# Performance work log

Measured on AMD Instinct MI355X. Metric: run time of the kernel, lower is better.

## Reference

```python
import jax, jax.numpy as jnp
import numpy as np

N = 4194304  # data_size
EPS = 1e-12  # torch f.normalize eps


def setup_inputs() -> dict:
    key = jax.random.key(0)
    k1, = jax.random.split(key, 1)
    inputs = jax.random.normal(k1, (N, 3, 3), dtype=jnp.float32)
    kd = jnp.zeros((3,), dtype=jnp.float32)   # nn.Parameter([0,0,0])
    ks = jnp.ones((3,), dtype=jnp.float32)    # nn.Parameter([1,1,1])
    p = jnp.float32(16.0)                     # nn.Parameter(16.0)
    return {"inputs": inputs, "kd": kd, "ks": ks, "p": p}


def reference(inputs, kd, ks, p):
    # inputs: [N, 3, 3] -> light, normal, view each [N, 3]
    light = inputs[:, 0, :]
    normal = inputs[:, 1, :]
    view = inputs[:, 2, :]
    intensity = jnp.float32(1.0)

    # diffuse: kd * intensity * max(0, dot(light, normal))  -> [N, 1] * [3]
    ln = jnp.maximum(0.0, jnp.sum(light * normal, axis=-1, keepdims=True))
    l_d = kd * intensity * ln  # [N, 3]

    # half vector: normalize(light + view) with torch's eps clamp on norm
    h = light + view
    norm = jnp.maximum(jnp.linalg.norm(h, axis=-1, keepdims=True), EPS)
    half = h / norm

    # specular: ks * intensity * max(0, dot(normal, half)) ** p
    nh = jnp.maximum(0.0, jnp.sum(normal * half, axis=-1, keepdims=True))
    l_s = ks * intensity * jnp.power(nh, p)  # [N, 3]

    return l_s + l_d  # [N, 3]
```

## Files before the change

### kernel.cpp

```cpp
#include <hip/hip_runtime.h>
#include <math.h>


#define BLOCK 256

__global__ __launch_bounds__(BLOCK) void blinn_phong_kernel(
    const float* __restrict__ in,
    const float* __restrict__ kd,
    const float* __restrict__ ks,
    const float* __restrict__ pp,
    float* __restrict__ out,
    int n)
{
    __shared__ float s_in[BLOCK * 9];
    __shared__ float s_out[BLOCK * 3];

    const int bid = blockIdx.x;
    const int tid = threadIdx.x;

    const long long blk_elem0 = (long long)bid * BLOCK;
    const float4* gin = (const float4*)(in + blk_elem0 * 9);
    float4* s4 = (float4*)s_in;
    const long long total4 = ((long long)n * 9) >> 2;
    const long long base4 = blk_elem0 * 9 / 4;
    if (base4 + tid < total4)       s4[tid]       = gin[tid];
    if (base4 + tid + 256 < total4) s4[tid + 256] = gin[tid + 256];
    if (tid < 64 && base4 + tid + 512 < total4) s4[tid + 512] = gin[tid + 512];
    __syncthreads();

    const long long elem = blk_elem0 + tid;
    if (elem < n) {
        const float* e = s_in + tid * 9;
        float Lx = e[0], Ly = e[1], Lz = e[2];
        float Nx = e[3], Ny = e[4], Nz = e[5];
        float Vx = e[6], Vy = e[7], Vz = e[8];

        float kd0 = kd[0], kd1 = kd[1], kd2 = kd[2];
        float ks0 = ks[0], ks1 = ks[1], ks2 = ks[2];
        float p = pp[0];

        float ln = fmaxf(0.0f, Lx * Nx + Ly * Ny + Lz * Nz);

        float hx = Lx + Vx, hy = Ly + Vy, hz = Lz + Vz;
        float hh = hx * hx + hy * hy + hz * hz;
        float inv = rsqrtf(fmaxf(hh, 1e-24f));

        float nh = fmaxf(0.0f, (Nx * hx + Ny * hy + Nz * hz) * inv);
        float spec = __builtin_amdgcn_exp2f(p * __builtin_amdgcn_logf(nh));

        s_out[tid * 3 + 0] = ks0 * spec + kd0 * ln;
        s_out[tid * 3 + 1] = ks1 * spec + kd1 * ln;
        s_out[tid * 3 + 2] = ks2 * spec + kd2 * ln;
    }
    __syncthreads();

    float4* gout = (float4*)(out + blk_elem0 * 3);
    const float4* so4 = (const float4*)s_out;
    const long long out_total4 = ((long long)n * 3) >> 2;
    const long long out_base4 = blk_elem0 * 3 / 4;
    if (tid < 192) {
        long long g = out_base4 + tid;
        if (g < out_total4) gout[tid] = so4[tid];
    }
}

extern "C" void kernel_launch(void* const* d_in, const int* in_sizes, int n_in,
                              void* d_out, int out_size, void* d_ws, size_t ws_size,
                              hipStream_t stream) {
    const float* in = (const float*)d_in[0];
    const float* kd = (const float*)d_in[1];
    const float* ks = (const float*)d_in[2];
    const float* pp = (const float*)d_in[3];
    float* out = (float*)d_out;

    int n = in_sizes[0] / 9;
    int grid = (n + BLOCK - 1) / BLOCK;
    blinn_phong_kernel<<<grid, BLOCK, 0, stream>>>(in, kd, ks, pp, out, n);
}
```

Baseline: 229.7 us.

## Process four elements per thread with batched register loads before LDS staging

Each block now handles 1024 elements instead of 256. All nine float4 global loads are issued into registers before any LDS store, so memory-level parallelism goes up. The shared buffer is reused for the output staging, with an extra barrier between compute and the output writes. The cost is a larger LDS footprint per block (36KB), which may lower occupancy, plus fewer blocks in the grid.

```diff
diff --git a/kernel.cpp b/kernel.cpp
--- a/kernel.cpp
+++ b/kernel.cpp
@@ -3,6 +3,8 @@
 
 
 #define BLOCK 256
+#define EPT 4
+#define TILE (BLOCK * EPT)
 
 __global__ __launch_bounds__(BLOCK) void blinn_phong_kernel(
     const float* __restrict__ in,
@@ -12,32 +14,36 @@
     float* __restrict__ out,
     int n)
 {
-    __shared__ float s_in[BLOCK * 9];
-    __shared__ float s_out[BLOCK * 3];
+    __shared__ float s_mem[TILE * 9];
 
-    const int bid = blockIdx.x;
     const int tid = threadIdx.x;
+    const long long blk0 = (long long)blockIdx.x * TILE;
 
-    const long long blk_elem0 = (long long)bid * BLOCK;
-    const float4* gin = (const float4*)(in + blk_elem0 * 9);
-    float4* s4 = (float4*)s_in;
+    const float4* gin = (const float4*)(in + blk0 * 9);
+    float4* s4 = (float4*)s_mem;
     const long long total4 = ((long long)n * 9) >> 2;
-    const long long base4 = blk_elem0 * 9 / 4;
-    if (base4 + tid < total4)       s4[tid]       = gin[tid];
-    if (base4 + tid + 256 < total4) s4[tid + 256] = gin[tid + 256];
-    if (tid < 64 && base4 + tid + 512 < total4) s4[tid + 512] = gin[tid + 512];
+    const long long base4 = blk0 * 9 / 4;
+    float4 r[9];
+#pragma unroll
+    for (int i = 0; i < 9; ++i) {
+        if (base4 + tid + i * BLOCK < total4) r[i] = gin[tid + i * BLOCK];
+    }
+#pragma unroll
+    for (int i = 0; i < 9; ++i) s4[tid + i * BLOCK] = r[i];
     __syncthreads();
 
-    const long long elem = blk_elem0 + tid;
-    if (elem < n) {
-        const float* e = s_in + tid * 9;
+    const float kd0 = kd[0], kd1 = kd[1], kd2 = kd[2];
+    const float ks0 = ks[0], ks1 = ks[1], ks2 = ks[2];
+    const float p = pp[0];
+
+    float o[EPT][3];
+#pragma unroll
+    for (int m = 0; m < EPT; ++m) {
+        const int j = tid + m * BLOCK;
+        const float* e = s_mem + j * 9;
         float Lx = e[0], Ly = e[1], Lz = e[2];
         float Nx = e[3], Ny = e[4], Nz = e[5];
         float Vx = e[6], Vy = e[7], Vz = e[8];
-
-        float kd0 = kd[0], kd1 = kd[1], kd2 = kd[2];
-        float ks0 = ks[0], ks1 = ks[1], ks2 = ks[2];
-        float p = pp[0];
 
         float ln = fmaxf(0.0f, Lx * Nx + Ly * Ny + Lz * Nz);
 
@@ -48,19 +54,28 @@
         float nh = fmaxf(0.0f, (Nx * hx + Ny * hy + Nz * hz) * inv);
         float spec = __builtin_amdgcn_exp2f(p * __builtin_amdgcn_logf(nh));
 
-        s_out[tid * 3 + 0] = ks0 * spec + kd0 * ln;
-        s_out[tid * 3 + 1] = ks1 * spec + kd1 * ln;
-        s_out[tid * 3 + 2] = ks2 * spec + kd2 * ln;
+        o[m][0] = ks0 * spec + kd0 * ln;
+        o[m][1] = ks1 * spec + kd1 * ln;
+        o[m][2] = ks2 * spec + kd2 * ln;
     }
     __syncthreads();
 
-    float4* gout = (float4*)(out + blk_elem0 * 3);
-    const float4* so4 = (const float4*)s_out;
+#pragma unroll
+    for (int m = 0; m < EPT; ++m) {
+        const int j = tid + m * BLOCK;
+        s_mem[3 * j + 0] = o[m][0];
+        s_mem[3 * j + 1] = o[m][1];
+        s_mem[3 * j + 2] = o[m][2];
+    }
+    __syncthreads();
+
+    float4* gout = (float4*)(out + blk0 * 3);
     const long long out_total4 = ((long long)n * 3) >> 2;
-    const long long out_base4 = blk_elem0 * 3 / 4;
-    if (tid < 192) {
-        long long g = out_base4 + tid;
-        if (g < out_total4) gout[tid] = so4[tid];
+    const long long out_base4 = blk0 * 3 / 4;
+#pragma unroll
+    for (int m = 0; m < 3; ++m) {
+        if (out_base4 + tid + m * BLOCK < out_total4)
+            gout[tid + m * BLOCK] = s4[tid + m * BLOCK];
     }
 }
 
@@ -74,6 +89,6 @@
     float* out = (float*)d_out;
 
     int n = in_sizes[0] / 9;
-    int grid = (n + BLOCK - 1) / BLOCK;
+    int grid = (n + TILE - 1) / TILE;
     blinn_phong_kernel<<<grid, BLOCK, 0, stream>>>(in, kd, ks, pp, out, n);
 }
```

New measurement: 261.8 us. 1.14x slower.
